# Kernel optimization log

Hardware: AMD Instinct MI355X
Metric: run time of the kernel (lower is better)

## Reference

```python
import jax, jax.numpy as jnp
import numpy as np

# Integrator: torchaudio lfilter with a=[1,-1], b=[1,0] ->
#   y[n] = x[n] + y[n-1]  (first-order IIR that is exactly a cumulative sum
#   along the time axis). We implement it directly as a parallel cumsum.

B, C, T = 8, 4, 1048576  # batch, channels, time (~65 s @ 16 kHz)

def setup_inputs() -> dict:
    key = jax.random.key(0)
    x = jax.random.normal(key, (B, C, T), dtype=jnp.float32)
    return {"x": x}

def reference(x):
    # lfilter recursion y[n] = x[n] + y[n-1] == cumulative sum over time axis
    return jnp.cumsum(x, axis=-1)
```

## Files before the change

### kernel.cpp

```cpp
#include <hip/hip_runtime.h>


constexpr int ROWS           = 32;
constexpr int T_LEN          = 1048576;
constexpr int THREADS        = 256;
constexpr int PER_THREAD     = 16;
constexpr int TILE           = THREADS * PER_THREAD;
constexpr int BLOCKS_PER_ROW = T_LEN / TILE;
constexpr int TOTAL_BLOCKS   = ROWS * BLOCKS_PER_ROW;

__global__ __launch_bounds__(THREADS) void integ_reduce(
    const float* __restrict__ x, float* __restrict__ part) {
  const int blk = blockIdx.x;
  const size_t base = (size_t)blk * TILE;
  const float4* p = (const float4*)(x + base);
  const int t = threadIdx.x;
  const int lane = t & 63;
  const int wid  = t >> 6;

  float s = 0.f;
#pragma unroll
  for (int j = 0; j < TILE / 4 / THREADS; ++j) {
    float4 v = p[j * THREADS + t];
    s += (v.x + v.y) + (v.z + v.w);
  }
#pragma unroll
  for (int d = 32; d > 0; d >>= 1) s += __shfl_down(s, d, 64);

  __shared__ float wsum[4];
  if (lane == 0) wsum[wid] = s;
  __syncthreads();
  if (t == 0) part[blk] = (wsum[0] + wsum[1]) + (wsum[2] + wsum[3]);
}

__global__ __launch_bounds__(THREADS) void integ_scan(
    const float* __restrict__ x, float* __restrict__ y,
    const float* __restrict__ part) {
  const int blk = blockIdx.x;
  const int row = blk >> 8;
  const int tb  = blk & (BLOCKS_PER_ROW - 1);
  const int t = threadIdx.x;
  const int lane = t & 63;
  const int wid  = t >> 6;

  __shared__ float s_pred[4];
  __shared__ float s_wscan[4];

  float ps = (t < tb) ? part[(row << 8) + t] : 0.f;
#pragma unroll
  for (int o = 32; o > 0; o >>= 1) ps += __shfl_xor(ps, o, 64);
  if (lane == 0) s_pred[wid] = ps;

  const size_t base = (size_t)blk * TILE + (size_t)t * PER_THREAD;
  const float4* p = (const float4*)(x + base);
  float v[PER_THREAD];
#pragma unroll
  for (int j = 0; j < PER_THREAD / 4; ++j) {
    float4 q = p[j];
    v[4 * j + 0] = q.x; v[4 * j + 1] = q.y; v[4 * j + 2] = q.z; v[4 * j + 3] = q.w;
  }

#pragma unroll
  for (int i = 1; i < PER_THREAD; ++i) v[i] += v[i - 1];
  const float tsum = v[PER_THREAD - 1];

  float s = tsum;
#pragma unroll
  for (int d = 1; d < 64; d <<= 1) {
    float n = __shfl_up(s, d, 64);
    if (lane >= d) s += n;
  }
  if (lane == 63) s_wscan[wid] = s;
  __syncthreads();

  float off = (s_pred[0] + s_pred[1]) + (s_pred[2] + s_pred[3]);
  float prev = 0.f;
#pragma unroll
  for (int w = 0; w < 4; ++w) prev += (w < wid) ? s_wscan[w] : 0.f;
  off += prev + s - tsum;

#pragma unroll
  for (int i = 0; i < PER_THREAD; ++i) v[i] += off;

  float4* q = (float4*)(y + base);
#pragma unroll
  for (int j = 0; j < PER_THREAD / 4; ++j) {
    float4 o;
    o.x = v[4 * j + 0]; o.y = v[4 * j + 1];
    o.z = v[4 * j + 2]; o.w = v[4 * j + 3];
    q[j] = o;
  }
}

extern "C" void kernel_launch(void* const* d_in, const int* in_sizes, int n_in,
                              void* d_out, int out_size, void* d_ws, size_t ws_size,
                              hipStream_t stream) {
  const float* x = (const float*)d_in[0];
  float* y = (float*)d_out;
  float* part = (float*)d_ws;

  integ_reduce<<<TOTAL_BLOCKS, THREADS, 0, stream>>>(x, part);
  integ_scan  <<<TOTAL_BLOCKS, THREADS, 0, stream>>>(x, y, part);
}
```

Baseline: 252.7 us.

## Fuse reduce and scan into one cooperative kernel with grid sync

Replaces the two-kernel reduce-then-scan with a single cooperative kernel. Each of 1024 blocks owns a 32K-element chunk: it reduces the chunk, the grid syncs, then it scans its chunk tile by tile while carrying a running total. The aim is to remove the second launch and to re-read each chunk soon enough that it may still be in cache. In exchange it depends on all 1024 blocks being co-resident for the grid sync, and it serialises tiles within each block.

```diff
diff --git a/kernel.cpp b/kernel.cpp
--- a/kernel.cpp
+++ b/kernel.cpp
@@ -1,94 +1,108 @@
 #include <hip/hip_runtime.h>
+#include <hip/hip_cooperative_groups.h>
 
+
+namespace cg = cooperative_groups;
 
 constexpr int ROWS           = 32;
 constexpr int T_LEN          = 1048576;
 constexpr int THREADS        = 256;
+constexpr int BLOCKS_PER_ROW = 32;
+constexpr int TOTAL_BLOCKS   = ROWS * BLOCKS_PER_ROW;
+constexpr int CHUNK          = T_LEN / BLOCKS_PER_ROW;
 constexpr int PER_THREAD     = 16;
 constexpr int TILE           = THREADS * PER_THREAD;
-constexpr int BLOCKS_PER_ROW = T_LEN / TILE;
-constexpr int TOTAL_BLOCKS   = ROWS * BLOCKS_PER_ROW;
+constexpr int TILES_PER_CHUNK = CHUNK / TILE;
 
-__global__ __launch_bounds__(THREADS) void integ_reduce(
-    const float* __restrict__ x, float* __restrict__ part) {
-  const int blk = blockIdx.x;
-  const size_t base = (size_t)blk * TILE;
-  const float4* p = (const float4*)(x + base);
-  const int t = threadIdx.x;
+__global__ __launch_bounds__(THREADS, 4) void integ_fused(
+    const float* __restrict__ x, float* __restrict__ y,
+    float* __restrict__ part) {
+  const int blk  = blockIdx.x;
+  const int row  = blk >> 5;
+  const int cb   = blk & 31;
+  const int t    = threadIdx.x;
   const int lane = t & 63;
   const int wid  = t >> 6;
 
-  float s = 0.f;
+  const size_t cbase = (size_t)blk * CHUNK;
+
+  __shared__ float s_red[4];
+
+  {
+    const float4* p = (const float4*)(x + cbase);
+    float s0 = 0.f, s1 = 0.f, s2 = 0.f, s3 = 0.f;
+#pragma unroll 2
+    for (int j = 0; j < CHUNK / 4 / THREADS; j += 4) {
+      float4 a = p[(j + 0) * THREADS + t];
+      float4 b = p[(j + 1) * THREADS + t];
+      float4 c = p[(j + 2) * THREADS + t];
+      float4 d = p[(j + 3) * THREADS + t];
+      s0 += (a.x + a.y) + (a.z + a.w);
+      s1 += (b.x + b.y) + (b.z + b.w);
+      s2 += (c.x + c.y) + (c.z + c.w);
+      s3 += (d.x + d.y) + (d.z + d.w);
+    }
+    float s = (s0 + s1) + (s2 + s3);
 #pragma unroll
-  for (int j = 0; j < TILE / 4 / THREADS; ++j) {
-    float4 v = p[j * THREADS + t];
-    s += (v.x + v.y) + (v.z + v.w);
+    for (int d = 32; d > 0; d >>= 1) s += __shfl_down(s, d, 64);
+    if (lane == 0) s_red[wid] = s;
+    __syncthreads();
+    if (t == 0) part[blk] = (s_red[0] + s_red[1]) + (s_red[2] + s_red[3]);
   }
-#pragma unroll
-  for (int d = 32; d > 0; d >>= 1) s += __shfl_down(s, d, 64);
 
-  __shared__ float wsum[4];
-  if (lane == 0) wsum[wid] = s;
-  __syncthreads();
-  if (t == 0) part[blk] = (wsum[0] + wsum[1]) + (wsum[2] + wsum[3]);
-}
+  cg::this_grid().sync();
 
-__global__ __launch_bounds__(THREADS) void integ_scan(
-    const float* __restrict__ x, float* __restrict__ y,
-    const float* __restrict__ part) {
-  const int blk = blockIdx.x;
-  const int row = blk >> 8;
-  const int tb  = blk & (BLOCKS_PER_ROW - 1);
-  const int t = threadIdx.x;
-  const int lane = t & 63;
-  const int wid  = t >> 6;
-
-  __shared__ float s_pred[4];
   __shared__ float s_wscan[4];
 
-  float ps = (t < tb) ? part[(row << 8) + t] : 0.f;
+  float ps = (lane < cb) ? part[(row << 5) + lane] : 0.f;
 #pragma unroll
   for (int o = 32; o > 0; o >>= 1) ps += __shfl_xor(ps, o, 64);
-  if (lane == 0) s_pred[wid] = ps;
+  float carry = ps;
 
-  const size_t base = (size_t)blk * TILE + (size_t)t * PER_THREAD;
-  const float4* p = (const float4*)(x + base);
-  float v[PER_THREAD];
+  for (int k = 0; k < TILES_PER_CHUNK; ++k) {
+    const size_t base = cbase + (size_t)k * TILE + (size_t)t * PER_THREAD;
+    const float4* p = (const float4*)(x + base);
+    float v[PER_THREAD];
 #pragma unroll
-  for (int j = 0; j < PER_THREAD / 4; ++j) {
-    float4 q = p[j];
-    v[4 * j + 0] = q.x; v[4 * j + 1] = q.y; v[4 * j + 2] = q.z; v[4 * j + 3] = q.w;
-  }
+    for (int j = 0; j < PER_THREAD / 4; ++j) {
+      float4 q = p[j];
+      v[4 * j + 0] = q.x; v[4 * j + 1] = q.y;
+      v[4 * j + 2] = q.z; v[4 * j + 3] = q.w;
+    }
 
 #pragma unroll
-  for (int i = 1; i < PER_THREAD; ++i) v[i] += v[i - 1];
-  const float tsum = v[PER_THREAD - 1];
+    for (int i = 1; i < PER_THREAD; ++i) v[i] += v[i - 1];
+    const float tsum = v[PER_THREAD - 1];
 
-  float s = tsum;
+    float s = tsum;
 #pragma unroll
-  for (int d = 1; d < 64; d <<= 1) {
-    float n = __shfl_up(s, d, 64);
-    if (lane >= d) s += n;
-  }
-  if (lane == 63) s_wscan[wid] = s;
-  __syncthreads();
+    for (int d = 1; d < 64; d <<= 1) {
+      float n = __shfl_up(s, d, 64);
+      if (lane >= d) s += n;
+    }
+    if (lane == 63) s_wscan[wid] = s;
+    __syncthreads();
 
-  float off = (s_pred[0] + s_pred[1]) + (s_pred[2] + s_pred[3]);
-  float prev = 0.f;
+    float off = carry + (s - tsum);
 #pragma unroll
-  for (int w = 0; w < 4; ++w) prev += (w < wid) ? s_wscan[w] : 0.f;
-  off += prev + s - tsum;
+    for (int w = 0; w < 4; ++w) off += (w < wid) ? s_wscan[w] : 0.f;
+    const float blockTotal =
+        (s_wscan[0] + s_wscan[1]) + (s_wscan[2] + s_wscan[3]);
 
 #pragma unroll
-  for (int i = 0; i < PER_THREAD; ++i) v[i] += off;
+    for (int i = 0; i < PER_THREAD; ++i) v[i] += off;
 
-  float4* q = (float4*)(y + base);
+    float4* q = (float4*)(y + base);
 #pragma unroll
-  for (int j = 0; j < PER_THREAD / 4; ++j) {
-    float4 o;
-    o.x = v[4 * j + 0]; o.y = v[4 * j + 1];
-    o.z = v[4 * j + 2]; o.w = v[4 * j + 3];
-    q[j] = o;
+    for (int j = 0; j < PER_THREAD / 4; ++j) {
+      float4 o;
+      o.x = v[4 * j + 0]; o.y = v[4 * j + 1];
+      o.z = v[4 * j + 2]; o.w = v[4 * j + 3];
+      q[j] = o;
+    }
+
+    carry += blockTotal;
+    __syncthreads();
   }
 }
 
@@ -99,6 +113,7 @@
   float* y = (float*)d_out;
   float* part = (float*)d_ws;
 
-  integ_reduce<<<TOTAL_BLOCKS, THREADS, 0, stream>>>(x, part);
-  integ_scan  <<<TOTAL_BLOCKS, THREADS, 0, stream>>>(x, y, part);
+  void* args[] = {(void*)&x, (void*)&y, (void*)&part};
+  hipLaunchCooperativeKernel((const void*)integ_fused, dim3(TOTAL_BLOCKS),
+                             dim3(THREADS), args, 0, stream);
 }
```

Result: slower. 372.1 us (+47.3%).

## Process four tiles per block with register prefetch and running carry

Applied to the files above, without the earlier changes.

Each block now handles four consecutive 4096-element tiles instead of one, in both the reduce and the scan kernels, which cuts the block count by four. The reduce kernel issues all loads up front and writes four partial sums. The scan kernel prefetches the next tile into registers while scanning the current one, and carries the running block total forward so the prefix over earlier tiles is computed only once per block. In exchange it uses more registers and fewer blocks, which may lower occupancy and latency hiding on a memory-bound scan.

```diff
diff --git a/kernel.cpp b/kernel.cpp
--- a/kernel.cpp
+++ b/kernel.cpp
@@ -6,89 +6,131 @@
 constexpr int THREADS        = 256;
 constexpr int PER_THREAD     = 16;
 constexpr int TILE           = THREADS * PER_THREAD;
-constexpr int BLOCKS_PER_ROW = T_LEN / TILE;
-constexpr int TOTAL_BLOCKS   = ROWS * BLOCKS_PER_ROW;
+constexpr int TILES_PER_ROW  = T_LEN / TILE;
+constexpr int TPG            = 4;
+constexpr int GROUPS_PER_ROW = TILES_PER_ROW / TPG;
+constexpr int TOTAL_GROUPS   = ROWS * GROUPS_PER_ROW;
 
 __global__ __launch_bounds__(THREADS) void integ_reduce(
     const float* __restrict__ x, float* __restrict__ part) {
-  const int blk = blockIdx.x;
-  const size_t base = (size_t)blk * TILE;
-  const float4* p = (const float4*)(x + base);
-  const int t = threadIdx.x;
+  const int blk  = blockIdx.x;
+  const int t    = threadIdx.x;
   const int lane = t & 63;
   const int wid  = t >> 6;
 
-  float s = 0.f;
+  const float4* p = (const float4*)(x + (size_t)blk * (TILE * TPG));
+
+  float4 q[TPG][4];
 #pragma unroll
-  for (int j = 0; j < TILE / 4 / THREADS; ++j) {
-    float4 v = p[j * THREADS + t];
-    s += (v.x + v.y) + (v.z + v.w);
+  for (int k = 0; k < TPG; ++k)
+#pragma unroll
+    for (int j = 0; j < 4; ++j)
+      q[k][j] = p[k * (TILE / 4) + j * THREADS + t];
+
+  float s[TPG];
+#pragma unroll
+  for (int k = 0; k < TPG; ++k) {
+    float a = (q[k][0].x + q[k][0].y) + (q[k][0].z + q[k][0].w);
+    float b = (q[k][1].x + q[k][1].y) + (q[k][1].z + q[k][1].w);
+    float c = (q[k][2].x + q[k][2].y) + (q[k][2].z + q[k][2].w);
+    float d = (q[k][3].x + q[k][3].y) + (q[k][3].z + q[k][3].w);
+    s[k] = (a + b) + (c + d);
   }
 #pragma unroll
-  for (int d = 32; d > 0; d >>= 1) s += __shfl_down(s, d, 64);
+  for (int k = 0; k < TPG; ++k)
+#pragma unroll
+    for (int o = 32; o > 0; o >>= 1) s[k] += __shfl_down(s[k], o, 64);
 
-  __shared__ float wsum[4];
-  if (lane == 0) wsum[wid] = s;
+  __shared__ float wsum[4][TPG];
+  if (lane == 0)
+#pragma unroll
+    for (int k = 0; k < TPG; ++k) wsum[wid][k] = s[k];
   __syncthreads();
-  if (t == 0) part[blk] = (wsum[0] + wsum[1]) + (wsum[2] + wsum[3]);
+  if (t < TPG)
+    part[blk * TPG + t] =
+        (wsum[0][t] + wsum[1][t]) + (wsum[2][t] + wsum[3][t]);
 }
 
 __global__ __launch_bounds__(THREADS) void integ_scan(
     const float* __restrict__ x, float* __restrict__ y,
     const float* __restrict__ part) {
-  const int blk = blockIdx.x;
-  const int row = blk >> 8;
-  const int tb  = blk & (BLOCKS_PER_ROW - 1);
-  const int t = threadIdx.x;
+  const int blk  = blockIdx.x;
+  const int row  = blk >> 6;
+  const int g    = blk & (GROUPS_PER_ROW - 1);
+  const int tb0  = g * TPG;
+  const int t    = threadIdx.x;
   const int lane = t & 63;
   const int wid  = t >> 6;
 
   __shared__ float s_pred[4];
-  __shared__ float s_wscan[4];
+  __shared__ float s_wscan[2][4];
 
-  float ps = (t < tb) ? part[(row << 8) + t] : 0.f;
+  float ps = (t < tb0) ? part[(row << 8) + t] : 0.f;
 #pragma unroll
   for (int o = 32; o > 0; o >>= 1) ps += __shfl_xor(ps, o, 64);
   if (lane == 0) s_pred[wid] = ps;
 
-  const size_t base = (size_t)blk * TILE + (size_t)t * PER_THREAD;
-  const float4* p = (const float4*)(x + base);
-  float v[PER_THREAD];
+  const float4* p = (const float4*)(x + (size_t)blk * (TILE * TPG));
+
+  float4 cur[4];
 #pragma unroll
-  for (int j = 0; j < PER_THREAD / 4; ++j) {
-    float4 q = p[j];
-    v[4 * j + 0] = q.x; v[4 * j + 1] = q.y; v[4 * j + 2] = q.z; v[4 * j + 3] = q.w;
-  }
+  for (int j = 0; j < 4; ++j) cur[j] = p[4 * t + j];
+
+  float carry = 0.f;
+#pragma unroll
+  for (int k = 0; k < TPG; ++k) {
+    float4 nxt[4];
+    if (k < TPG - 1) {
+#pragma unroll
+      for (int j = 0; j < 4; ++j)
+        nxt[j] = p[(k + 1) * (TILE / 4) + 4 * t + j];
+    }
+
+    float v[PER_THREAD];
+#pragma unroll
+    for (int j = 0; j < 4; ++j) {
+      v[4 * j + 0] = cur[j].x; v[4 * j + 1] = cur[j].y;
+      v[4 * j + 2] = cur[j].z; v[4 * j + 3] = cur[j].w;
+    }
 
 #pragma unroll
-  for (int i = 1; i < PER_THREAD; ++i) v[i] += v[i - 1];
-  const float tsum = v[PER_THREAD - 1];
+    for (int i = 1; i < PER_THREAD; ++i) v[i] += v[i - 1];
+    const float tsum = v[PER_THREAD - 1];
 
-  float s = tsum;
+    float s = tsum;
 #pragma unroll
-  for (int d = 1; d < 64; d <<= 1) {
-    float n = __shfl_up(s, d, 64);
-    if (lane >= d) s += n;
-  }
-  if (lane == 63) s_wscan[wid] = s;
-  __syncthreads();
+    for (int d = 1; d < 64; d <<= 1) {
+      float n = __shfl_up(s, d, 64);
+      if (lane >= d) s += n;
+    }
+    if (lane == 63) s_wscan[k & 1][wid] = s;
+    __syncthreads();
 
-  float off = (s_pred[0] + s_pred[1]) + (s_pred[2] + s_pred[3]);
-  float prev = 0.f;
+    if (k == 0)
+      carry = (s_pred[0] + s_pred[1]) + (s_pred[2] + s_pred[3]);
+
+    float off = carry + (s - tsum);
 #pragma unroll
-  for (int w = 0; w < 4; ++w) prev += (w < wid) ? s_wscan[w] : 0.f;
-  off += prev + s - tsum;
+    for (int w = 0; w < 4; ++w) off += (w < wid) ? s_wscan[k & 1][w] : 0.f;
+    const float blockTotal = (s_wscan[k & 1][0] + s_wscan[k & 1][1]) +
+                             (s_wscan[k & 1][2] + s_wscan[k & 1][3]);
 
 #pragma unroll
-  for (int i = 0; i < PER_THREAD; ++i) v[i] += off;
+    for (int i = 0; i < PER_THREAD; ++i) v[i] += off;
 
-  float4* q = (float4*)(y + base);
+    float4* qo = (float4*)((float*)(y + (size_t)blk * (TILE * TPG)) +
+                           k * TILE + 16 * t);
 #pragma unroll
-  for (int j = 0; j < PER_THREAD / 4; ++j) {
-    float4 o;
-    o.x = v[4 * j + 0]; o.y = v[4 * j + 1];
-    o.z = v[4 * j + 2]; o.w = v[4 * j + 3];
-    q[j] = o;
+    for (int j = 0; j < 4; ++j) {
+      float4 o;
+      o.x = v[4 * j + 0]; o.y = v[4 * j + 1];
+      o.z = v[4 * j + 2]; o.w = v[4 * j + 3];
+      qo[j] = o;
+    }
+
+    carry += blockTotal;
+#pragma unroll
+    for (int j = 0; j < 4; ++j) cur[j] = nxt[j];
   }
 }
 
@@ -99,6 +141,6 @@
   float* y = (float*)d_out;
   float* part = (float*)d_ws;
 
-  integ_reduce<<<TOTAL_BLOCKS, THREADS, 0, stream>>>(x, part);
-  integ_scan  <<<TOTAL_BLOCKS, THREADS, 0, stream>>>(x, y, part);
+  integ_reduce<<<TOTAL_GROUPS, THREADS, 0, stream>>>(x, part);
+  integ_scan  <<<TOTAL_GROUPS, THREADS, 0, stream>>>(x, y, part);
 }
```

New measurement: 261.0 us. +3.3%, slower.
